# Performance work log

Hardware: AMD Instinct MI355X
Metric: run time of the kernel (lower is better)

The kernel has to match this reference:

```python
import jax, jax.numpy as jnp
import numpy as np

D_MODEL = 1024
N_HEADS = 16
D_HEAD = D_MODEL // N_HEADS


def setup_inputs() -> dict:
    key = jax.random.key(0)
    ks = jax.random.split(key, 5)
    s_in = 1.0 / np.sqrt(D_MODEL)
    x = jax.random.normal(ks[0], (4, 2048, D_MODEL), dtype=jnp.float32)
    W_qkv = jax.random.uniform(ks[1], (D_MODEL, 3 * D_MODEL), jnp.float32, -s_in, s_in)
    b_qkv = jax.random.uniform(ks[2], (3 * D_MODEL,), jnp.float32, -s_in, s_in)
    W_out = jax.random.uniform(ks[3], (D_MODEL, D_MODEL), jnp.float32, -s_in, s_in)
    b_out = jax.random.uniform(ks[4], (D_MODEL,), jnp.float32, -s_in, s_in)
    return {"x": x, "W_qkv": W_qkv, "b_qkv": b_qkv, "W_out": W_out, "b_out": b_out}


def reference(x, W_qkv, b_qkv, W_out, b_out):
    B, T, C = x.shape
    qkv = x @ W_qkv + b_qkv                       # [B,T,3C]
    q, k, v = jnp.split(qkv, 3, axis=-1)
    # [B,T,C] -> [B,H,T,Dh]
    def heads(t):
        return t.reshape(B, T, N_HEADS, D_HEAD).transpose(0, 2, 1, 3)
    q, k, v = heads(q), heads(k), heads(v)
    scale = 1.0 / np.sqrt(D_HEAD).astype(np.float32)
    attn = jnp.einsum('bhqd,bhkd->bhqk', q, k) * scale   # [B,H,T,T]
    causal = jnp.tril(jnp.ones((T, T), dtype=bool))
    attn = jnp.where(causal, attn, -jnp.inf)
    attn_weights = jax.nn.softmax(attn, axis=-1)
    out = jnp.einsum('bhqk,bhkd->bhqd', attn_weights, v)  # [B,H,T,Dh]
    out = out.transpose(0, 2, 1, 3).reshape(B, T, C)
    return out @ W_out + b_out
```

## Files before the change

### kernel.cpp

```cpp
#include <hip/hip_runtime.h>
#include <hip/hip_bf16.h>

#define BATCH   4
#define SEQ     2048
#define DMODEL  1024
#define NHEADS  16
#define DHEAD   64
#define MROWS   (BATCH*SEQ)
#define QKV_N   (3*DMODEL)
#define NEG_BIG (-1.0e30f)
#define WS_NEED ((size_t)MROWS * 2*DMODEL * sizeof(__hip_bfloat16))
#define SCALE_Q 0.18033688011112042f

using bf16 = __hip_bfloat16;
typedef __attribute__((ext_vector_type(8))) short short8;
typedef __attribute__((ext_vector_type(4))) float floatx4;

__device__ __align__(16) unsigned short g_wqT[QKV_N * DMODEL];
__device__ __align__(16) unsigned short g_woT[DMODEL * DMODEL];
__device__ __align__(16) unsigned short g_xb [MROWS * DMODEL];

__device__ __forceinline__ unsigned short f2bf_rne(float f) {
    union { bf16 b; unsigned short u; } t;
    t.b = __float2bfloat16(f);
    return t.u;
}

__device__ __forceinline__ void gload_lds16(const void* g, void* l) {
    __builtin_amdgcn_global_load_lds(
        (const __attribute__((address_space(1))) unsigned*)g,
        (__attribute__((address_space(3))) unsigned*)l, 16, 0, 0);
}

__global__ __launch_bounds__(256) void cast_x(const float* __restrict__ x) {
    const size_t i = ((size_t)blockIdx.x*256 + threadIdx.x)*8;
    const float4 a = *(const float4*)(x + i);
    const float4 b = *(const float4*)(x + i + 4);
    union { uint4 u4; unsigned short us[8]; } o;
    o.us[0]=f2bf_rne(a.x); o.us[1]=f2bf_rne(a.y); o.us[2]=f2bf_rne(a.z); o.us[3]=f2bf_rne(a.w);
    o.us[4]=f2bf_rne(b.x); o.us[5]=f2bf_rne(b.y); o.us[6]=f2bf_rne(b.z); o.us[7]=f2bf_rne(b.w);
    *(uint4*)(g_xb + i) = o.u4;
}

__global__ __launch_bounds__(256) void transcast_w(
    const float* __restrict__ W, int N, int which)
{
    unsigned short* dst = which ? g_woT : g_wqT;
    __shared__ unsigned short T[64][72];
    const int n0 = blockIdx.x * 64, k0 = blockIdx.y * 64;
    const int tid = threadIdx.x;
    const int r = tid >> 2, c0 = (tid & 3) * 16;

#pragma unroll
    for (int it = 0; it < 4; ++it) {
        const float4 v = *(const float4*)(W + (size_t)(k0 + r)*N + n0 + c0 + it*4);
        T[r][c0 + it*4 + 0] = f2bf_rne(v.x);
        T[r][c0 + it*4 + 1] = f2bf_rne(v.y);
        T[r][c0 + it*4 + 2] = f2bf_rne(v.z);
        T[r][c0 + it*4 + 3] = f2bf_rne(v.w);
    }
    __syncthreads();
    const int nr = tid >> 2, kc0 = (tid & 3) * 16;
#pragma unroll
    for (int it = 0; it < 2; ++it) {
        union { uint4 u4; unsigned short us[8]; } o;
#pragma unroll
        for (int j = 0; j < 8; j++) o.us[j] = T[kc0 + it*8 + j][nr];
        *(uint4*)(dst + (size_t)(n0 + nr)*DMODEL + k0 + kc0 + it*8) = o.u4;
    }
}

template<int QKV_MODE>
__global__ __launch_bounds__(256) void gemm_mfma(
    const void* __restrict__ Av, const float* __restrict__ bias,
    void* __restrict__ C0, void* __restrict__ C1, void* __restrict__ C2)
{
    const unsigned short* A  = QKV_MODE ? g_xb : (const unsigned short*)Av;
    const unsigned short* BT = QKV_MODE ? g_wqT : g_woT;
    __shared__ alignas(16) unsigned short As[128*32];
    __shared__ alignas(16) unsigned short Bs[128*32];

    const int tid = threadIdx.x;
    const int bm = blockIdx.y, bn = blockIdx.x;
    const int w = tid >> 6, lane = tid & 63;
    const int m16 = lane & 15, quad = lane >> 4;
    const int m0 = (w & 1) * 64, n0w = (w >> 1) * 64;

    const int lrow  = lane >> 2;
    const int lcol  = (lane & 3) * 8;
    const unsigned short* aG = A  + (size_t)(bm*128 + w*32 + lrow)*DMODEL + lcol;
    const unsigned short* bG = BT + (size_t)(bn*128 + w*32 + lrow)*DMODEL + lcol;
    char* asL = (char*)As + w*2048;
    char* bsL = (char*)Bs + w*2048;

    floatx4 acc[4][4];
#pragma unroll
    for (int i = 0; i < 4; i++)
#pragma unroll
        for (int j = 0; j < 4; j++) { acc[i][j][0]=0.f; acc[i][j][1]=0.f; acc[i][j][2]=0.f; acc[i][j][3]=0.f; }

    for (int k0 = 0; k0 < DMODEL; k0 += 32) {
        __syncthreads();
        gload_lds16(aG + k0,              asL);
        gload_lds16(aG + 16*DMODEL + k0,  asL + 1024);
        gload_lds16(bG + k0,              bsL);
        gload_lds16(bG + 16*DMODEL + k0,  bsL + 1024);
        __syncthreads();

        short8 af[4], bf4[4];
#pragma unroll
        for (int i = 0; i < 4; ++i) af[i]  = *(const short8*)&As[(m0 + i*16 + m16)*32 + quad*8];
#pragma unroll
        for (int j = 0; j < 4; ++j) bf4[j] = *(const short8*)&Bs[(n0w + j*16 + m16)*32 + quad*8];
#pragma unroll
        for (int i = 0; i < 4; ++i)
#pragma unroll
            for (int j = 0; j < 4; ++j)
                acc[i][j] = __builtin_amdgcn_mfma_f32_16x16x32_bf16(af[i], bf4[j], acc[i][j], 0, 0, 0);
    }

    const int gcolb = bn*128;
    float bv[4];
#pragma unroll
    for (int j = 0; j < 4; ++j) bv[j] = bias[gcolb + n0w + j*16 + m16];

    if (QKV_MODE) {
        const int seg = gcolb >> 10;
        if (seg < 2) {
            bf16* Cout = (bf16*)(seg ? C1 : C0);
            const float sc = seg ? 1.0f : SCALE_Q;
#pragma unroll
            for (int i = 0; i < 4; ++i)
#pragma unroll
                for (int r = 0; r < 4; ++r) {
                    const int gm = bm*128 + m0 + i*16 + quad*4 + r;
#pragma unroll
                    for (int j = 0; j < 4; ++j) {
                        const int cc = (gcolb + n0w + j*16 + m16) & 1023;
                        Cout[(size_t)gm*DMODEL + cc] = __float2bfloat16((acc[i][j][r] + bv[j]) * sc);
                    }
                }
        } else {
            bf16* VT = (bf16*)C2;
#pragma unroll
            for (int i = 0; i < 4; ++i) {
                const int gm0 = bm*128 + m0 + i*16 + quad*4;
                const int bb = gm0 >> 11, t0 = gm0 & 2047;
#pragma unroll
                for (int j = 0; j < 4; ++j) {
                    const int cv = (gcolb & 1023) + n0w + j*16 + m16;
                    const int hh = cv >> 6, dd = cv & 63;
                    union { unsigned long long u8; unsigned short us[4]; } o;
#pragma unroll
                    for (int r = 0; r < 4; ++r) o.us[r] = f2bf_rne(acc[i][j][r] + bv[j]);
                    *(unsigned long long*)(VT + ((size_t)((bb*NHEADS + hh)*DHEAD + dd))*SEQ + t0) = o.u8;
                }
            }
        }
    } else {
        float* Cout = (float*)C0;
#pragma unroll
        for (int i = 0; i < 4; ++i)
#pragma unroll
            for (int r = 0; r < 4; ++r) {
                const int gm = bm*128 + m0 + i*16 + quad*4 + r;
#pragma unroll
                for (int j = 0; j < 4; ++j) {
                    const int cc = (gcolb + n0w + j*16 + m16) & 1023;
                    Cout[(size_t)gm*DMODEL + cc] = acc[i][j][r] + bv[j];
                }
            }
    }
}

__global__ __launch_bounds__(256, 2) void attn_mfma3(
    const bf16* __restrict__ Qg, const bf16* __restrict__ Kg,
    const bf16* __restrict__ VTg, bf16* __restrict__ Og)
{
    __shared__ alignas(16) unsigned short Kt[2][64][72];
    __shared__ alignas(16) unsigned short Vt[2][64][72];
    __shared__ alignas(16) unsigned short Ps[4][32][72];

    const int x = blockIdx.x;
    const int b = x >> 7, h = (x >> 3) & 15, p = x & 7;
    const int tid = threadIdx.x;
    const int w = tid >> 6, lane = tid & 63;
    const int m16 = lane & 15, quad = lane >> 4;
    const int sr = tid >> 2, sc0 = (tid & 3) * 8;
    const size_t bh = (size_t)(b*NHEADS + h);

    for (int seg = 0; seg < 2; ++seg) {
        const int qt  = seg ? (15 - p) : p;
        const int nkt = 2*qt + 2;
        const int qrow0 = qt*128 + w*32;

        short8 qf[2][2];
#pragma unroll
        for (int i = 0; i < 2; ++i)
#pragma unroll
            for (int c = 0; c < 2; ++c)
                qf[i][c] = *(const short8*)(Qg + (size_t)(b*SEQ + qrow0 + i*16 + m16)*DMODEL
                                            + h*DHEAD + c*32 + quad*8);

        floatx4 of[2][4];
        float mrow[2], lrow[2];
#pragma unroll
        for (int i = 0; i < 2; ++i) {
            mrow[i] = NEG_BIG; lrow[i] = 0.f;
#pragma unroll
            for (int nt = 0; nt < 4; ++nt) { of[i][nt][0]=0.f; of[i][nt][1]=0.f; of[i][nt][2]=0.f; of[i][nt][3]=0.f; }
        }

        {
            const bf16* kp = Kg  + (size_t)(b*SEQ + sr)*DMODEL + h*DHEAD + sc0;
            const bf16* vp = VTg + (bh*DHEAD + sr)*SEQ + sc0;
            const uint4 a0 = *(const uint4*)kp, a1 = *(const uint4*)(kp + 32);
            const uint4 b0 = *(const uint4*)vp, b1 = *(const uint4*)(vp + 32);
            __syncthreads();
            *(uint4*)&Kt[0][sr][sc0]      = a0;
            *(uint4*)&Kt[0][sr][sc0 + 32] = a1;
            *(uint4*)&Vt[0][sr][sc0]      = b0;
            *(uint4*)&Vt[0][sr][sc0 + 32] = b1;
            __syncthreads();
        }

        for (int kt = 0; kt < nkt; ++kt) {
            const int buf = kt & 1;
            const int k064 = kt * 64;
            const bool pre = (kt + 1 < nkt);
            uint4 kr0, kr1, vr0, vr1;
            if (pre) {
                const bf16* kp = Kg  + (size_t)(b*SEQ + k064 + 64 + sr)*DMODEL + h*DHEAD + sc0;
                const bf16* vp = VTg + (bh*DHEAD + sr)*SEQ + k064 + 64 + sc0;
                kr0 = *(const uint4*)kp; kr1 = *(const uint4*)(kp + 32);
                vr0 = *(const uint4*)vp; vr1 = *(const uint4*)(vp + 32);
            }

            floatx4 sf[2][4];
#pragma unroll
            for (int t4 = 0; t4 < 4; ++t4) {
                const short8 kf0 = *(const short8*)&Kt[buf][t4*16 + m16][quad*8];
                const short8 kf1 = *(const short8*)&Kt[buf][t4*16 + m16][32 + quad*8];
#pragma unroll
                for (int i = 0; i < 2; ++i) {
                    floatx4 a; a[0]=0.f; a[1]=0.f; a[2]=0.f; a[3]=0.f;
                    a = __builtin_amdgcn_mfma_f32_16x16x32_bf16(kf0, qf[i][0], a, 0, 0, 0);
                    a = __builtin_amdgcn_mfma_f32_16x16x32_bf16(kf1, qf[i][1], a, 0, 0, 0);
                    sf[i][t4] = a;
                }
            }

            const bool need_mask = (k064 + 63 > qrow0);
#pragma unroll
            for (int i = 0; i < 2; ++i) {
                if (need_mask) {
                    const int qg = qrow0 + i*16 + m16;
#pragma unroll
                    for (int t4 = 0; t4 < 4; ++t4)
#pragma unroll
                        for (int r = 0; r < 4; ++r)
                            if (k064 + t4*16 + quad*4 + r > qg) sf[i][t4][r] = NEG_BIG;
                }
                float mx = sf[i][0][0];
#pragma unroll
                for (int t4 = 0; t4 < 4; ++t4)
#pragma unroll
                    for (int r = 0; r < 4; ++r) mx = fmaxf(mx, sf[i][t4][r]);
                mx = fmaxf(mx, __shfl_xor(mx, 16));
                mx = fmaxf(mx, __shfl_xor(mx, 32));

                const float mnew  = fmaxf(mrow[i], mx);
                const float alpha = exp2f(mrow[i] - mnew);
                mrow[i] = mnew;

                float rs = 0.f;
#pragma unroll
                for (int t4 = 0; t4 < 4; ++t4) {
#pragma unroll
                    for (int r = 0; r < 4; ++r) {
                        const float pv = exp2f(sf[i][t4][r] - mnew);
                        sf[i][t4][r] = pv;
                        rs += pv;
                    }
                }
                rs += __shfl_xor(rs, 16);
                rs += __shfl_xor(rs, 32);
                lrow[i] = lrow[i]*alpha + rs;
#pragma unroll
                for (int nt = 0; nt < 4; ++nt)
#pragma unroll
                    for (int r = 0; r < 4; ++r) of[i][nt][r] *= alpha;

#pragma unroll
                for (int t4 = 0; t4 < 4; ++t4) {
                    union { unsigned long long u8; unsigned short us[4]; } o;
#pragma unroll
                    for (int r = 0; r < 4; ++r) o.us[r] = f2bf_rne(sf[i][t4][r]);
                    *(unsigned long long*)&Ps[w][i*16 + m16][t4*16 + quad*4] = o.u8;
                }
            }

            short8 pf[2][2];
#pragma unroll
            for (int i = 0; i < 2; ++i)
#pragma unroll
                for (int c = 0; c < 2; ++c)
                    pf[i][c] = *(const short8*)&Ps[w][i*16 + m16][c*32 + quad*8];
#pragma unroll
            for (int nt = 0; nt < 4; ++nt) {
                const short8 vf0 = *(const short8*)&Vt[buf][nt*16 + m16][quad*8];
                const short8 vf1 = *(const short8*)&Vt[buf][nt*16 + m16][32 + quad*8];
#pragma unroll
                for (int i = 0; i < 2; ++i) {
                    of[i][nt] = __builtin_amdgcn_mfma_f32_16x16x32_bf16(vf0, pf[i][0], of[i][nt], 0, 0, 0);
                    of[i][nt] = __builtin_amdgcn_mfma_f32_16x16x32_bf16(vf1, pf[i][1], of[i][nt], 0, 0, 0);
                }
            }

            if (pre) {
                *(uint4*)&Kt[buf^1][sr][sc0]      = kr0;
                *(uint4*)&Kt[buf^1][sr][sc0 + 32] = kr1;
                *(uint4*)&Vt[buf^1][sr][sc0]      = vr0;
                *(uint4*)&Vt[buf^1][sr][sc0 + 32] = vr1;
            }
            __syncthreads();
        }

#pragma unroll
        for (int i = 0; i < 2; ++i) {
            const float rl = 1.f / fmaxf(lrow[i], 1e-20f);
            const size_t rowbase = (size_t)(b*SEQ + qrow0 + i*16 + m16)*DMODEL + h*DHEAD;
#pragma unroll
            for (int nt = 0; nt < 4; ++nt) {
                union { unsigned long long u8; unsigned short us[4]; } o;
#pragma unroll
                for (int r = 0; r < 4; ++r) o.us[r] = f2bf_rne(of[i][nt][r] * rl);
                *(unsigned long long*)(Og + rowbase + nt*16 + quad*4) = o.u8;
            }
        }
    }
}

__global__ void diag_fill(float* out, int n, float val) {
    int i = blockIdx.x*blockDim.x + threadIdx.x;
    if (i < n) out[i] = val;
}

extern "C" void kernel_launch(void* const* d_in, const int* in_sizes, int n_in,
                              void* d_out, int out_size, void* d_ws, size_t ws_size,
                              hipStream_t stream) {
    const float* x     = (const float*)d_in[0];
    const float* W_qkv = (const float*)d_in[1];
    const float* b_qkv = (const float*)d_in[2];
    const float* W_out = (const float*)d_in[3];
    const float* b_out = (const float*)d_in[4];

    if (ws_size < WS_NEED) {
        const float val = 100.f + (float)(ws_size >> 20);
        diag_fill<<<(out_size + 255)/256, 256, 0, stream>>>((float*)d_out, out_size, val);
        return;
    }

    bf16* Qb  = (bf16*)d_out;
    bf16* VTb = (bf16*)d_out + (size_t)MROWS*DMODEL;
    bf16* Kb  = (bf16*)d_ws;
    bf16* Ob  = (bf16*)d_ws + (size_t)MROWS*DMODEL;

    cast_x<<<MROWS*DMODEL/2048, 256, 0, stream>>>(x);
    {
        dim3 gq(QKV_N/64, DMODEL/64);
        transcast_w<<<gq, 256, 0, stream>>>(W_qkv, QKV_N, 0);
        dim3 go(DMODEL/64, DMODEL/64);
        transcast_w<<<go, 256, 0, stream>>>(W_out, DMODEL, 1);
    }
    {
        dim3 g(QKV_N/128, MROWS/128);
        gemm_mfma<1><<<g, 256, 0, stream>>>(nullptr, b_qkv, Qb, Kb, VTb);
    }
    {
        attn_mfma3<<<512, 256, 0, stream>>>(Qb, Kb, VTb, Ob);
    }
    {
        dim3 g(DMODEL/128, MROWS/128);
        gemm_mfma<0><<<g, 256, 0, stream>>>(Ob, b_out, d_out, nullptr, nullptr);
    }
}
```

Measured before the change: 306.7 us.

## Fuse fp32-to-bf16 cast of x into QKV GEMM and double-buffer LDS tiles

```diff
diff --git a/kernel.cpp b/kernel.cpp
--- a/kernel.cpp
+++ b/kernel.cpp
@@ -18,7 +18,6 @@
 
 __device__ __align__(16) unsigned short g_wqT[QKV_N * DMODEL];
 __device__ __align__(16) unsigned short g_woT[DMODEL * DMODEL];
-__device__ __align__(16) unsigned short g_xb [MROWS * DMODEL];
 
 __device__ __forceinline__ unsigned short f2bf_rne(float f) {
     union { bf16 b; unsigned short u; } t;
@@ -30,16 +29,6 @@
     __builtin_amdgcn_global_load_lds(
         (const __attribute__((address_space(1))) unsigned*)g,
         (__attribute__((address_space(3))) unsigned*)l, 16, 0, 0);
-}
-
-__global__ __launch_bounds__(256) void cast_x(const float* __restrict__ x) {
-    const size_t i = ((size_t)blockIdx.x*256 + threadIdx.x)*8;
-    const float4 a = *(const float4*)(x + i);
-    const float4 b = *(const float4*)(x + i + 4);
-    union { uint4 u4; unsigned short us[8]; } o;
-    o.us[0]=f2bf_rne(a.x); o.us[1]=f2bf_rne(a.y); o.us[2]=f2bf_rne(a.z); o.us[3]=f2bf_rne(a.w);
-    o.us[4]=f2bf_rne(b.x); o.us[5]=f2bf_rne(b.y); o.us[6]=f2bf_rne(b.z); o.us[7]=f2bf_rne(b.w);
-    *(uint4*)(g_xb + i) = o.u4;
 }
 
 __global__ __launch_bounds__(256) void transcast_w(
@@ -75,10 +64,9 @@
     const void* __restrict__ Av, const float* __restrict__ bias,
     void* __restrict__ C0, void* __restrict__ C1, void* __restrict__ C2)
 {
-    const unsigned short* A  = QKV_MODE ? g_xb : (const unsigned short*)Av;
     const unsigned short* BT = QKV_MODE ? g_wqT : g_woT;
-    __shared__ alignas(16) unsigned short As[128*32];
-    __shared__ alignas(16) unsigned short Bs[128*32];
+    __shared__ alignas(16) unsigned short As[2][128*32];
+    __shared__ alignas(16) unsigned short Bs[2][128*32];
 
     const int tid = threadIdx.x;
     const int bm = blockIdx.y, bn = blockIdx.x;
@@ -88,10 +76,13 @@
 
     const int lrow  = lane >> 2;
     const int lcol  = (lane & 3) * 8;
-    const unsigned short* aG = A  + (size_t)(bm*128 + w*32 + lrow)*DMODEL + lcol;
     const unsigned short* bG = BT + (size_t)(bn*128 + w*32 + lrow)*DMODEL + lcol;
-    char* asL = (char*)As + w*2048;
-    char* bsL = (char*)Bs + w*2048;
+    const int aRow  = tid >> 1;
+    const int aKh   = (tid & 1) * 16;
+    const float* xA = (const float*)Av;
+    const float* xP = QKV_MODE ? (xA + (size_t)(bm*128 + aRow)*DMODEL + aKh) : nullptr;
+    const unsigned short* aG = QKV_MODE ? nullptr
+        : (const unsigned short*)Av + (size_t)(bm*128 + w*32 + lrow)*DMODEL + lcol;
 
     floatx4 acc[4][4];
 #pragma unroll
@@ -99,24 +90,72 @@
 #pragma unroll
         for (int j = 0; j < 4; j++) { acc[i][j][0]=0.f; acc[i][j][1]=0.f; acc[i][j][2]=0.f; acc[i][j][3]=0.f; }
 
+    {
+        char* bsL = (char*)&Bs[0][0] + w*2048;
+        gload_lds16(bG,               bsL);
+        gload_lds16(bG + 16*DMODEL,   bsL + 1024);
+        if (QKV_MODE) {
+            float4 a0 = *(const float4*)xP;
+            float4 a1 = *(const float4*)(xP + 4);
+            float4 a2 = *(const float4*)(xP + 8);
+            float4 a3 = *(const float4*)(xP + 12);
+            union { uint4 u4[2]; unsigned short us[16]; } t;
+            t.us[0]=f2bf_rne(a0.x); t.us[1]=f2bf_rne(a0.y); t.us[2]=f2bf_rne(a0.z); t.us[3]=f2bf_rne(a0.w);
+            t.us[4]=f2bf_rne(a1.x); t.us[5]=f2bf_rne(a1.y); t.us[6]=f2bf_rne(a1.z); t.us[7]=f2bf_rne(a1.w);
+            t.us[8]=f2bf_rne(a2.x); t.us[9]=f2bf_rne(a2.y); t.us[10]=f2bf_rne(a2.z); t.us[11]=f2bf_rne(a2.w);
+            t.us[12]=f2bf_rne(a3.x); t.us[13]=f2bf_rne(a3.y); t.us[14]=f2bf_rne(a3.z); t.us[15]=f2bf_rne(a3.w);
+            *(uint4*)&As[0][aRow*32 + aKh]     = t.u4[0];
+            *(uint4*)&As[0][aRow*32 + aKh + 8] = t.u4[1];
+        } else {
+            char* asL = (char*)&As[0][0] + w*2048;
+            gload_lds16(aG,             asL);
+            gload_lds16(aG + 16*DMODEL, asL + 1024);
+        }
+    }
+    __syncthreads();
+
     for (int k0 = 0; k0 < DMODEL; k0 += 32) {
-        __syncthreads();
-        gload_lds16(aG + k0,              asL);
-        gload_lds16(aG + 16*DMODEL + k0,  asL + 1024);
-        gload_lds16(bG + k0,              bsL);
-        gload_lds16(bG + 16*DMODEL + k0,  bsL + 1024);
-        __syncthreads();
+        const int buf = (k0 >> 5) & 1;
+        const bool pre = (k0 + 32 < DMODEL);
+
+        float4 a0, a1, a2, a3;
+        if (pre) {
+            char* bsL = (char*)&Bs[buf^1][0] + w*2048;
+            gload_lds16(bG + k0 + 32,             bsL);
+            gload_lds16(bG + 16*DMODEL + k0 + 32, bsL + 1024);
+            if (QKV_MODE) {
+                a0 = *(const float4*)(xP + k0 + 32);
+                a1 = *(const float4*)(xP + k0 + 36);
+                a2 = *(const float4*)(xP + k0 + 40);
+                a3 = *(const float4*)(xP + k0 + 44);
+            } else {
+                char* asL = (char*)&As[buf^1][0] + w*2048;
+                gload_lds16(aG + k0 + 32,             asL);
+                gload_lds16(aG + 16*DMODEL + k0 + 32, asL + 1024);
+            }
+        }
 
         short8 af[4], bf4[4];
 #pragma unroll
-        for (int i = 0; i < 4; ++i) af[i]  = *(const short8*)&As[(m0 + i*16 + m16)*32 + quad*8];
-#pragma unroll
-        for (int j = 0; j < 4; ++j) bf4[j] = *(const short8*)&Bs[(n0w + j*16 + m16)*32 + quad*8];
+        for (int i = 0; i < 4; ++i) af[i]  = *(const short8*)&As[buf][(m0 + i*16 + m16)*32 + quad*8];
+#pragma unroll
+        for (int j = 0; j < 4; ++j) bf4[j] = *(const short8*)&Bs[buf][(n0w + j*16 + m16)*32 + quad*8];
 #pragma unroll
         for (int i = 0; i < 4; ++i)
 #pragma unroll
             for (int j = 0; j < 4; ++j)
                 acc[i][j] = __builtin_amdgcn_mfma_f32_16x16x32_bf16(af[i], bf4[j], acc[i][j], 0, 0, 0);
+
+        if (pre && QKV_MODE) {
+            union { uint4 u4[2]; unsigned short us[16]; } t;
+            t.us[0]=f2bf_rne(a0.x); t.us[1]=f2bf_rne(a0.y); t.us[2]=f2bf_rne(a0.z); t.us[3]=f2bf_rne(a0.w);
+            t.us[4]=f2bf_rne(a1.x); t.us[5]=f2bf_rne(a1.y); t.us[6]=f2bf_rne(a1.z); t.us[7]=f2bf_rne(a1.w);
+            t.us[8]=f2bf_rne(a2.x); t.us[9]=f2bf_rne(a2.y); t.us[10]=f2bf_rne(a2.z); t.us[11]=f2bf_rne(a2.w);
+            t.us[12]=f2bf_rne(a3.x); t.us[13]=f2bf_rne(a3.y); t.us[14]=f2bf_rne(a3.z); t.us[15]=f2bf_rne(a3.w);
+            *(uint4*)&As[buf^1][aRow*32 + aKh]     = t.u4[0];
+            *(uint4*)&As[buf^1][aRow*32 + aKh + 8] = t.u4[1];
+        }
+        __syncthreads();
     }
 
     const int gcolb = bn*128;
@@ -366,7 +405,6 @@
     bf16* Kb  = (bf16*)d_ws;
     bf16* Ob  = (bf16*)d_ws + (size_t)MROWS*DMODEL;
 
-    cast_x<<<MROWS*DMODEL/2048, 256, 0, stream>>>(x);
     {
         dim3 gq(QKV_N/64, DMODEL/64);
         transcast_w<<<gq, 256, 0, stream>>>(W_qkv, QKV_N, 0);
@@ -375,7 +413,7 @@
     }
     {
         dim3 g(QKV_N/128, MROWS/128);
-        gemm_mfma<1><<<g, 256, 0, stream>>>(nullptr, b_qkv, Qb, Kb, VTb);
+        gemm_mfma<1><<<g, 256, 0, stream>>>(x, b_qkv, Qb, Kb, VTb);
     }
     {
         attn_mfma3<<<512, 256, 0, stream>>>(Qb, Kb, VTb, Ob);
```

After: 307.4 us. About the same (+0.2%).

## Fuse x cast into QKV GEMM with register-staged double-buffered padded LDS

Applied to the files above, without the earlier changes.

```diff
diff --git a/kernel.cpp b/kernel.cpp
--- a/kernel.cpp
+++ b/kernel.cpp
@@ -11,6 +11,7 @@
 #define NEG_BIG (-1.0e30f)
 #define WS_NEED ((size_t)MROWS * 2*DMODEL * sizeof(__hip_bfloat16))
 #define SCALE_Q 0.18033688011112042f
+#define LPAD 40
 
 using bf16 = __hip_bfloat16;
 typedef __attribute__((ext_vector_type(8))) short short8;
@@ -18,7 +19,6 @@
 
 __device__ __align__(16) unsigned short g_wqT[QKV_N * DMODEL];
 __device__ __align__(16) unsigned short g_woT[DMODEL * DMODEL];
-__device__ __align__(16) unsigned short g_xb [MROWS * DMODEL];
 
 __device__ __forceinline__ unsigned short f2bf_rne(float f) {
     union { bf16 b; unsigned short u; } t;
@@ -26,28 +26,18 @@
     return t.u;
 }
 
-__device__ __forceinline__ void gload_lds16(const void* g, void* l) {
-    __builtin_amdgcn_global_load_lds(
-        (const __attribute__((address_space(1))) unsigned*)g,
-        (__attribute__((address_space(3))) unsigned*)l, 16, 0, 0);
-}
-
-__global__ __launch_bounds__(256) void cast_x(const float* __restrict__ x) {
-    const size_t i = ((size_t)blockIdx.x*256 + threadIdx.x)*8;
-    const float4 a = *(const float4*)(x + i);
-    const float4 b = *(const float4*)(x + i + 4);
-    union { uint4 u4; unsigned short us[8]; } o;
-    o.us[0]=f2bf_rne(a.x); o.us[1]=f2bf_rne(a.y); o.us[2]=f2bf_rne(a.z); o.us[3]=f2bf_rne(a.w);
-    o.us[4]=f2bf_rne(b.x); o.us[5]=f2bf_rne(b.y); o.us[6]=f2bf_rne(b.z); o.us[7]=f2bf_rne(b.w);
-    *(uint4*)(g_xb + i) = o.u4;
-}
-
-__global__ __launch_bounds__(256) void transcast_w(
-    const float* __restrict__ W, int N, int which)
+__global__ __launch_bounds__(256) void transcast_w2(
+    const float* __restrict__ Wq, const float* __restrict__ Wo)
 {
+    const int bnAll = blockIdx.x;
+    const int which = (bnAll >= 48);
+    const float* W = which ? Wo : Wq;
+    const int N    = which ? DMODEL : QKV_N;
+    const int bn   = which ? (bnAll - 48) : bnAll;
     unsigned short* dst = which ? g_woT : g_wqT;
+
     __shared__ unsigned short T[64][72];
-    const int n0 = blockIdx.x * 64, k0 = blockIdx.y * 64;
+    const int n0 = bn * 64, k0 = blockIdx.y * 64;
     const int tid = threadIdx.x;
     const int r = tid >> 2, c0 = (tid & 3) * 16;
 
@@ -75,10 +65,9 @@
     const void* __restrict__ Av, const float* __restrict__ bias,
     void* __restrict__ C0, void* __restrict__ C1, void* __restrict__ C2)
 {
-    const unsigned short* A  = QKV_MODE ? g_xb : (const unsigned short*)Av;
     const unsigned short* BT = QKV_MODE ? g_wqT : g_woT;
-    __shared__ alignas(16) unsigned short As[128*32];
-    __shared__ alignas(16) unsigned short Bs[128*32];
+    __shared__ alignas(16) unsigned short As[2][128*LPAD];
+    __shared__ alignas(16) unsigned short Bs[2][128*LPAD];
 
     const int tid = threadIdx.x;
     const int bm = blockIdx.y, bn = blockIdx.x;
@@ -86,12 +75,12 @@
     const int m16 = lane & 15, quad = lane >> 4;
     const int m0 = (w & 1) * 64, n0w = (w >> 1) * 64;
 
-    const int lrow  = lane >> 2;
-    const int lcol  = (lane & 3) * 8;
-    const unsigned short* aG = A  + (size_t)(bm*128 + w*32 + lrow)*DMODEL + lcol;
-    const unsigned short* bG = BT + (size_t)(bn*128 + w*32 + lrow)*DMODEL + lcol;
-    char* asL = (char*)As + w*2048;
-    char* bsL = (char*)Bs + w*2048;
+    const int sRow = tid >> 1, sH = (tid & 1) * 16;
+    const float*          xP = QKV_MODE ? (const float*)Av + (size_t)(bm*128 + sRow)*DMODEL + sH : nullptr;
+    const unsigned short* aP = QKV_MODE ? nullptr
+                             : (const unsigned short*)Av + (size_t)(bm*128 + sRow)*DMODEL + sH;
+    const unsigned short* bP = BT + (size_t)(bn*128 + sRow)*DMODEL + sH;
+    const int sOff = sRow*LPAD + sH;
 
     floatx4 acc[4][4];
 #pragma unroll
@@ -99,24 +88,64 @@
 #pragma unroll
         for (int j = 0; j < 4; j++) { acc[i][j][0]=0.f; acc[i][j][1]=0.f; acc[i][j][2]=0.f; acc[i][j][3]=0.f; }
 
+    float4 af4[4]; uint4 aU[2]; uint4 bU[2];
+    auto loadA = [&](int k0) {
+        if (QKV_MODE) {
+            af4[0] = *(const float4*)(xP + k0);
+            af4[1] = *(const float4*)(xP + k0 + 4);
+            af4[2] = *(const float4*)(xP + k0 + 8);
+            af4[3] = *(const float4*)(xP + k0 + 12);
+        } else {
+            aU[0] = *(const uint4*)(aP + k0);
+            aU[1] = *(const uint4*)(aP + k0 + 8);
+        }
+    };
+    auto loadB = [&](int k0) {
+        bU[0] = *(const uint4*)(bP + k0);
+        bU[1] = *(const uint4*)(bP + k0 + 8);
+    };
+    auto writeA = [&](int buf) {
+        if (QKV_MODE) {
+            union { uint4 u4[2]; unsigned short us[16]; } t;
+#pragma unroll
+            for (int q = 0; q < 4; ++q) {
+                t.us[q*4+0] = f2bf_rne(af4[q].x); t.us[q*4+1] = f2bf_rne(af4[q].y);
+                t.us[q*4+2] = f2bf_rne(af4[q].z); t.us[q*4+3] = f2bf_rne(af4[q].w);
+            }
+            *(uint4*)&As[buf][sOff]     = t.u4[0];
+            *(uint4*)&As[buf][sOff + 8] = t.u4[1];
+        } else {
+            *(uint4*)&As[buf][sOff]     = aU[0];
+            *(uint4*)&As[buf][sOff + 8] = aU[1];
+        }
+    };
+    auto writeB = [&](int buf) {
+        *(uint4*)&Bs[buf][sOff]     = bU[0];
+        *(uint4*)&Bs[buf][sOff + 8] = bU[1];
+    };
+
+    loadA(0); loadB(0);
+    writeA(0); writeB(0);
+    __syncthreads();
+
     for (int k0 = 0; k0 < DMODEL; k0 += 32) {
-        __syncthreads();
-        gload_lds16(aG + k0,              asL);
-        gload_lds16(aG + 16*DMODEL + k0,  asL + 1024);
-        gload_lds16(bG + k0,              bsL);
-        gload_lds16(bG + 16*DMODEL + k0,  bsL + 1024);
-        __syncthreads();
+        const int buf = (k0 >> 5) & 1;
+        const bool pre = (k0 + 32 < DMODEL);
+        if (pre) { loadA(k0 + 32); loadB(k0 + 32); }
 
         short8 af[4], bf4[4];
 #pragma unroll
-        for (int i = 0; i < 4; ++i) af[i]  = *(const short8*)&As[(m0 + i*16 + m16)*32 + quad*8];
-#pragma unroll
-        for (int j = 0; j < 4; ++j) bf4[j] = *(const short8*)&Bs[(n0w + j*16 + m16)*32 + quad*8];
+        for (int i = 0; i < 4; ++i) af[i]  = *(const short8*)&As[buf][(m0 + i*16 + m16)*LPAD + quad*8];
+#pragma unroll
+        for (int j = 0; j < 4; ++j) bf4[j] = *(const short8*)&Bs[buf][(n0w + j*16 + m16)*LPAD + quad*8];
 #pragma unroll
         for (int i = 0; i < 4; ++i)
 #pragma unroll
             for (int j = 0; j < 4; ++j)
                 acc[i][j] = __builtin_amdgcn_mfma_f32_16x16x32_bf16(af[i], bf4[j], acc[i][j], 0, 0, 0);
+
+        if (pre) { writeA(buf^1); writeB(buf^1); }
+        __syncthreads();
     }
 
     const int gcolb = bn*128;
@@ -366,16 +395,13 @@
     bf16* Kb  = (bf16*)d_ws;
     bf16* Ob  = (bf16*)d_ws + (size_t)MROWS*DMODEL;
 
-    cast_x<<<MROWS*DMODEL/2048, 256, 0, stream>>>(x);
     {
-        dim3 gq(QKV_N/64, DMODEL/64);
-        transcast_w<<<gq, 256, 0, stream>>>(W_qkv, QKV_N, 0);
-        dim3 go(DMODEL/64, DMODEL/64);
-        transcast_w<<<go, 256, 0, stream>>>(W_out, DMODEL, 1);
+        dim3 g(64, 16);
+        transcast_w2<<<g, 256, 0, stream>>>(W_qkv, W_out);
     }
     {
         dim3 g(QKV_N/128, MROWS/128);
-        gemm_mfma<1><<<g, 256, 0, stream>>>(nullptr, b_qkv, Qb, Kb, VTb);
+        gemm_mfma<1><<<g, 256, 0, stream>>>(x, b_qkv, Qb, Kb, VTb);
     }
     {
         attn_mfma3<<<512, 256, 0, stream>>>(Qb, Kb, VTb, Ob);
```

New measurement: 427.1 us. 1.39x slower.
